# Kernel optimization log

Hardware: AMD Instinct MI355X
Metric: run time of the kernel (lower is better)

Reference implementation:

```python
import jax, jax.numpy as jnp
import numpy as np

B, T, V, D = 64, 128, 50000, 1024  # batch, num_steps, vocab_size, size


def setup_inputs() -> dict:
    key = jax.random.key(0)
    ks = jax.random.split(key, 5)
    inputs = jax.random.randint(ks[0], (B, T), 0, V, dtype=jnp.int32)
    input_lengths = jax.random.randint(ks[1], (B,), 0, T, dtype=jnp.int32)
    emb = jax.random.normal(ks[2], (V, D), dtype=jnp.float32) * 0.1  # ~truncated_normal(-0.1,0.1)
    # BasicLSTMCell weights: [input_dim + hidden, 4*hidden]
    W1 = jax.random.normal(ks[3], (2 * D, 4 * D), dtype=jnp.float32) / np.sqrt(2 * D)
    b1 = jnp.zeros((4 * D,), dtype=jnp.float32)
    W2 = jax.random.normal(ks[4], (2 * D, 4 * D), dtype=jnp.float32) / np.sqrt(2 * D)
    b2 = jnp.zeros((4 * D,), dtype=jnp.float32)
    return {"inputs": inputs, "input_lengths": input_lengths,
            "emb": emb, "W1": W1, "b1": b1, "W2": W2, "b2": b2}


def _lstm_cell(c, h, x, W, b):
    # BasicLSTMCell with forget_bias=0.0
    gates = jnp.concatenate([x, h], axis=-1) @ W + b  # [B, 4D]
    i, j, f, o = jnp.split(gates, 4, axis=-1)
    c_new = c * jax.nn.sigmoid(f) + jax.nn.sigmoid(i) * jnp.tanh(j)
    h_new = jnp.tanh(c_new) * jax.nn.sigmoid(o)
    return c_new, h_new


def reference(inputs, input_lengths, emb, W1, b1, W2, b2):
    # embedding_lookup on transposed inputs -> time-major [T, B, D]
    x_seq = jnp.transpose(emb[inputs], (1, 0, 2))
    # sequence_length semantics of tf rnn.rnn: past length, output is zero
    # and state is carried through unchanged.
    mask = (jnp.arange(T)[:, None] < input_lengths[None, :]).astype(emb.dtype)  # [T, B]

    def step(carry, xm):
        c1, h1, c2, h2 = carry
        x_t, m_t = xm
        m = m_t[:, None]  # [B, 1]
        c1n, h1n = _lstm_cell(c1, h1, x_t, W1, b1)
        c2n, h2n = _lstm_cell(c2, h2, h1n, W2, b2)
        c1 = m * c1n + (1.0 - m) * c1
        h1 = m * h1n + (1.0 - m) * h1
        c2 = m * c2n + (1.0 - m) * c2
        h2 = m * h2n + (1.0 - m) * h2
        out_t = h2n * m  # zero output past sequence end
        return (c1, h1, c2, h2), out_t

    zeros = jnp.zeros((B, D), dtype=emb.dtype)
    init = (zeros, zeros, zeros, zeros)
    _, outs = jax.lax.scan(step, init, (x_seq, mask))  # outs: [T, B, D]
    return outs.sum(axis=0)  # reduce_sum over time -> [B, D]
```

## Files before the change

kernel.cpp:

```cpp
#include <hip/hip_runtime.h>

#define B_ 64
#define T_ 128
#define D_ 1024
#define K2_ 2048
#define G_ 4096
#define SLOTW 65664

typedef __attribute__((ext_vector_type(8))) short bf16x8;
typedef __attribute__((ext_vector_type(4))) float f32x4;
typedef unsigned short u16;
typedef unsigned long long u64;

__device__ __forceinline__ u16 f2bf(float f) {
  unsigned int u = __float_as_uint(f);
  u += 0x7FFF + ((u >> 16) & 1);
  return (u16)(u >> 16);
}

__device__ __forceinline__ float fast_sigmoid(float x) {
  return 1.f / (1.f + __expf(-x));
}
__device__ __forceinline__ float fast_tanh(float x) {
  float e = __expf(-2.f * fabsf(x));
  float t = (1.f - e) / (1.f + e);
  return copysignf(t, x);
}

__device__ __forceinline__ void store4_wt(u16* addr, unsigned v) {
  asm volatile("global_store_dword %0, %1, off sc0 sc1"
               :: "v"((void*)addr), "v"(v) : "memory");
}

__device__ __forceinline__ void store_pair_wt(u16* base, size_t soff, u16 v, int tid) {
  unsigned other = __shfl_xor((unsigned)v, 1);
  if (!(tid & 1))
    store4_wt(base + soff, (unsigned)v | (other << 16));
}

__global__ __launch_bounds__(256) void transpose_w(const float* __restrict__ W,
                                                   u16* __restrict__ Wt) {
  __shared__ u16 tile[64][65];
  int bn = blockIdx.x & 63;
  int bk = blockIdx.x >> 6;
  int n0 = bn * 64, k0 = bk * 64;
  for (int i = threadIdx.x; i < 4096; i += 256) {
    int r = i >> 6, c = i & 63;
    tile[c][r] = f2bf(W[(size_t)(k0 + r) * G_ + n0 + c]);
  }
  __syncthreads();
  for (int i = threadIdx.x; i < 4096; i += 256) {
    int r = i >> 6, c = i & 63;
    Wt[(size_t)(n0 + r) * K2_ + k0 + c] = tile[r][c];
  }
}

__global__ __launch_bounds__(256) void gather_x(const int* __restrict__ inputs,
                                                const float* __restrict__ emb,
                                                u16* __restrict__ xg) {
  int idx = blockIdx.x * 256 + threadIdx.x;
  int d4 = idx & 255;
  int tb = idx >> 8;
  int t = tb >> 6, b = tb & 63;
  int tok = inputs[b * T_ + t];
  float4 v = ((const float4*)(emb + (size_t)tok * D_))[d4];
  u64 pk = (u64)f2bf(v.x)
         | ((u64)f2bf(v.y) << 16)
         | ((u64)f2bf(v.z) << 32)
         | ((u64)f2bf(v.w) << 48);
  *(u64*)(xg + (size_t)tb * D_ + d4 * 4) = pk;
}

__global__ void zero_buf(uint4* p, int n) {
  int i = blockIdx.x * blockDim.x + threadIdx.x;
  if (i < n) p[i] = make_uint4(0u, 0u, 0u, 0u);
}

__device__ __forceinline__ void arrive_dev(int* bar, int lineBase, int lb) {
  int a = __hip_atomic_fetch_add(bar + (size_t)(lineBase + (lb & 7)) * 32, 1,
                                 __ATOMIC_RELAXED, __HIP_MEMORY_SCOPE_AGENT);
  if (a == 15) {
    int r = __hip_atomic_fetch_add(bar + (size_t)(lineBase + 8) * 32, 1,
                                   __ATOMIC_RELAXED, __HIP_MEMORY_SCOPE_AGENT);
    if (r == 7)
      __hip_atomic_store(bar + (size_t)(lineBase + 9) * 32, 1,
                         __ATOMIC_RELAXED, __HIP_MEMORY_SCOPE_AGENT);
  }
}
__device__ __forceinline__ void waitdone_dev(int* bar, int lineBase) {
  while (!__hip_atomic_load(bar + (size_t)(lineBase + 9) * 32,
                            __ATOMIC_RELAXED, __HIP_MEMORY_SCOPE_AGENT))
    __builtin_amdgcn_s_sleep(1);
}
#define LINEOF(L, i) (10 + ((L) * 129 + (i)) * 10)

__global__ __launch_bounds__(512, 2) void lstm_persist(
    const u16* wt1, const u16* wt2,
    const u16* __restrict__ xg,
    u16* h1buf, u16* h1n, u16* h2buf,
    const u16* __restrict__ zbuf,
    const float* __restrict__ b1, const float* __restrict__ b2,
    const int* __restrict__ lens, float* __restrict__ out,
    int* bar) {
  __shared__ __attribute__((aligned(16))) float part[8][64][36];
  __shared__ __attribute__((aligned(16))) float gsum[64][36];
  const int blk = blockIdx.x;
  const int L = blk >> 7;
  const int lb = blk & 127;
  const int rg = lb & 1;
  const int cg = lb >> 1;
  const int tid = threadIdx.x;
  const int lane = tid & 63;
  const int wv = tid >> 6;
  const int dc = lane & 15;
  const int kq = lane >> 4;

  const u16* wt = L ? wt2 : wt1;
  const float* bias = L ? b2 : b1;

  bf16x8 wreg[4][8];
  {
    const u16* wb = wt + (size_t)(cg * 16 + dc) * K2_ + wv * 256 + kq * 8;
    #pragma unroll
    for (int g = 0; g < 4; ++g)
      #pragma unroll
      for (int ks = 0; ks < 8; ++ks)
        wreg[g][ks] = *(const bf16x8*)(wb + (size_t)g * D_ * K2_ + ks * 32);
  }
  #pragma unroll
  for (int g = 0; g < 4; ++g)
    #pragma unroll
    for (int ks = 0; ks < 8; ++ks)
      asm volatile("" : "+v"(wreg[g][ks]));

  const int crow = tid >> 4;
  const int cdc = tid & 15;
  const int grow = rg * 32 + crow;
  const int dcol = cg * 16 + cdc;
  const int len_r = lens[grow];
  float bias_g[4];
  #pragma unroll
  for (int g = 0; g < 4; ++g) bias_g[g] = bias[g * D_ + dcol];
  float creg = 0.f, hreg = 0.f, outreg = 0.f;

  const int r0 = rg * 32 + (lane & 15);
  const int koff = (wv & 3) * 256 + kq * 8;

  __syncthreads();
  if (tid == 0) {
    int a = __hip_atomic_fetch_add(bar + (size_t)(blk & 7) * 32, 1,
                                   __ATOMIC_RELAXED, __HIP_MEMORY_SCOPE_AGENT);
    if (a == 31) {
      int r = __hip_atomic_fetch_add(bar + 8 * 32, 1,
                                     __ATOMIC_RELAXED, __HIP_MEMORY_SCOPE_AGENT);
      if (r == 7)
        __hip_atomic_store(bar + 9 * 32, 1,
                           __ATOMIC_RELAXED, __HIP_MEMORY_SCOPE_AGENT);
    }
    while (!__hip_atomic_load(bar + 9 * 32,
                              __ATOMIC_RELAXED, __HIP_MEMORY_SCOPE_AGENT))
      __builtin_amdgcn_s_sleep(1);
  }
  __syncthreads();
  __builtin_amdgcn_fence(__ATOMIC_ACQUIRE, "agent");

  for (int i = 0; i <= 128; ++i) {
    const bool active = L ? (i >= 1) : (i < 128);
    const int t = L ? i - 1 : i;
    if (active) {
      if (tid == 0) {
        if (L == 0) {
          if (i >= 1) waitdone_dev(bar, LINEOF(0, i - 1));
        } else {
          waitdone_dev(bar, LINEOF(0, i - 1));
          if (i >= 2) waitdone_dev(bar, LINEOF(1, i - 1));
        }
      }
      __syncthreads();

      const u16* xsrc; const u16* hsrc;
      u16* w_h1n = nullptr; u16* w_h1b = nullptr; u16* w_h2b = nullptr;
      if (L == 0) {
        xsrc = xg + (size_t)t * (B_ * D_);
        hsrc = (i == 0) ? zbuf : h1buf + (size_t)(i - 1) * SLOTW;
        w_h1n = h1n + (size_t)i * SLOTW;
        w_h1b = h1buf + (size_t)i * SLOTW;
      } else {
        xsrc = h1n + (size_t)(i - 1) * SLOTW;
        hsrc = (i <= 1) ? zbuf : h2buf + (size_t)(i - 2) * SLOTW;
        w_h2b = h2buf + (size_t)(i - 1) * SLOTW;
      }
      const u16* src = (wv < 4) ? xsrc : hsrc;
      const u16* a0p = src + (size_t)r0 * D_ + koff;

      f32x4 acc[2][4];
      #pragma unroll
      for (int rt = 0; rt < 2; ++rt)
        #pragma unroll
        for (int g = 0; g < 4; ++g)
          acc[rt][g] = (f32x4){0.f, 0.f, 0.f, 0.f};

      #pragma unroll
      for (int ks = 0; ks < 8; ++ks) {
        bf16x8 a0 = *(const bf16x8*)(a0p + ks * 32);
        bf16x8 a1 = *(const bf16x8*)(a0p + 16 * D_ + ks * 32);
        #pragma unroll
        for (int g = 0; g < 4; ++g) {
          acc[0][g] = __builtin_amdgcn_mfma_f32_16x16x32_bf16(a0, wreg[g][ks], acc[0][g], 0, 0, 0);
          acc[1][g] = __builtin_amdgcn_mfma_f32_16x16x32_bf16(a1, wreg[g][ks], acc[1][g], 0, 0, 0);
        }
      }

      #pragma unroll
      for (int rt = 0; rt < 2; ++rt)
        #pragma unroll
        for (int g = 0; g < 4; ++g)
          *(f32x4*)&part[wv][g * 16 + dc][rt * 16 + kq * 4] = acc[rt][g];
      __syncthreads();

      {
        const int rcol = tid >> 3;
        const int rrow = (tid & 7) * 4;
        f32x4 s = *(const f32x4*)&part[0][rcol][rrow];
        #pragma unroll
        for (int w = 1; w < 8; ++w) s += *(const f32x4*)&part[w][rcol][rrow];
        *(f32x4*)&gsum[rcol][rrow] = s;
      }
      __syncthreads();

      {
        float gi = gsum[cdc][crow] + bias_g[0];
        float gj = gsum[16 + cdc][crow] + bias_g[1];
        float gf = gsum[32 + cdc][crow] + bias_g[2];
        float go = gsum[48 + cdc][crow] + bias_g[3];
        float is = fast_sigmoid(gi);
        float fs = fast_sigmoid(gf);
        float os = fast_sigmoid(go);
        float jt = fast_tanh(gj);
        float c_new = creg * fs + is * jt;
        float h_new = fast_tanh(c_new) * os;
        bool m = t < len_r;
        if (m) { creg = c_new; hreg = h_new; }
        size_t soff = (size_t)grow * D_ + dcol;
        if (L == 0) {
          store_pair_wt(w_h1n, soff, f2bf(h_new), tid);
          store_pair_wt(w_h1b, soff, f2bf(hreg), tid);
        } else {
          store_pair_wt(w_h2b, soff, f2bf(hreg), tid);
          if (m) outreg += h_new;
        }
      }

      asm volatile("s_waitcnt vmcnt(0)" ::: "memory");
      __syncthreads();
      if (tid == 0 && !(L == 1 && i == 128))
        arrive_dev(bar, LINEOF(L, i), lb);
    }
  }
  if (L == 1) out[(size_t)grow * D_ + dcol] = outreg;
}

extern "C" void kernel_launch(void* const* d_in, const int* in_sizes, int n_in,
                              void* d_out, int out_size, void* d_ws, size_t ws_size,
                              hipStream_t stream) {
  const int* inputs  = (const int*)d_in[0];
  const int* lengths = (const int*)d_in[1];
  const float* emb   = (const float*)d_in[2];
  const float* W1    = (const float*)d_in[3];
  const float* b1    = (const float*)d_in[4];
  const float* W2    = (const float*)d_in[5];
  const float* b2    = (const float*)d_in[6];
  float* out = (float*)d_out;

  char* p = (char*)d_ws;
  u16* h1buf = (u16*)p; p += (size_t)T_ * SLOTW * 2;
  u16* h1n   = (u16*)p; p += (size_t)T_ * SLOTW * 2;
  u16* h2buf = (u16*)p; p += (size_t)T_ * SLOTW * 2;
  u16* xg    = (u16*)p; p += (size_t)T_ * B_ * D_ * 2;
  u16* zbuf  = (u16*)p; p += (size_t)B_ * D_ * 2;
  int* bar   = (int*)p; p += 2590 * 128;
  u16* wt1 = h1buf;
  u16* wt2 = h1n;

  hipLaunchKernelGGL(transpose_w, dim3(2048), dim3(256), 0, stream, W1, wt1);
  hipLaunchKernelGGL(transpose_w, dim3(2048), dim3(256), 0, stream, W2, wt2);
  hipLaunchKernelGGL(gather_x, dim3(8192), dim3(256), 0, stream, inputs, emb, xg);
  hipLaunchKernelGGL(zero_buf, dim3(113), dim3(256), 0, stream, (uint4*)zbuf, 28912);

  hipLaunchKernelGGL(lstm_persist, dim3(256), dim3(512), 0, stream,
                     wt1, wt2, xg, h1buf, h1n, h2buf, zbuf, b1, b2, lengths, out,
                     bar);
}
```

Measured before the change: 921.2 us.

## Replace global barrier tree with XCD-local counters and per-XCD byte flags

Each block now counts arrivals on a counter local to its XCD (read from the hardware XCC id register). The last arriver on each XCD writes a byte flag, and waiters poll one 64-bit word of flags masked by the XCDs that are populated. This replaces the two-level agent-scope atomic tree plus done flag that every step paid, aiming to cut cross-die atomic latency on the per-timestep critical path. It relies on the workgroup-scope atomic being coherent among blocks on the same XCD, and on the XCD population counts being stable after the initial barrier.

```diff
diff --git a/kernel.cpp b/kernel.cpp
--- a/kernel.cpp
+++ b/kernel.cpp
@@ -27,8 +27,18 @@
   return copysignf(t, x);
 }
 
+__device__ __forceinline__ int get_xcc_id() {
+  int x;
+  asm volatile("s_getreg_b32 %0, hwreg(HW_REG_XCC_ID)" : "=s"(x));
+  return x & 7;
+}
+
 __device__ __forceinline__ void store4_wt(u16* addr, unsigned v) {
   asm volatile("global_store_dword %0, %1, off sc0 sc1"
+               :: "v"((void*)addr), "v"(v) : "memory");
+}
+__device__ __forceinline__ void store1_wt(unsigned char* addr, unsigned v) {
+  asm volatile("global_store_byte %0, %1, off sc0 sc1"
                :: "v"((void*)addr), "v"(v) : "memory");
 }
 
@@ -76,23 +86,7 @@
   if (i < n) p[i] = make_uint4(0u, 0u, 0u, 0u);
 }
 
-__device__ __forceinline__ void arrive_dev(int* bar, int lineBase, int lb) {
-  int a = __hip_atomic_fetch_add(bar + (size_t)(lineBase + (lb & 7)) * 32, 1,
-                                 __ATOMIC_RELAXED, __HIP_MEMORY_SCOPE_AGENT);
-  if (a == 15) {
-    int r = __hip_atomic_fetch_add(bar + (size_t)(lineBase + 8) * 32, 1,
-                                   __ATOMIC_RELAXED, __HIP_MEMORY_SCOPE_AGENT);
-    if (r == 7)
-      __hip_atomic_store(bar + (size_t)(lineBase + 9) * 32, 1,
-                         __ATOMIC_RELAXED, __HIP_MEMORY_SCOPE_AGENT);
-  }
-}
-__device__ __forceinline__ void waitdone_dev(int* bar, int lineBase) {
-  while (!__hip_atomic_load(bar + (size_t)(lineBase + 9) * 32,
-                            __ATOMIC_RELAXED, __HIP_MEMORY_SCOPE_AGENT))
-    __builtin_amdgcn_s_sleep(1);
-}
-#define LINEOF(L, i) (10 + ((L) * 129 + (i)) * 10)
+#define LOCLINE(L, x, i) (26 + ((L) * 8 + (x)) * 128 + (i))
 
 __global__ __launch_bounds__(512, 2) void lstm_persist(
     const u16* wt1, const u16* wt2,
@@ -101,7 +95,7 @@
     const u16* __restrict__ zbuf,
     const float* __restrict__ b1, const float* __restrict__ b2,
     const int* __restrict__ lens, float* __restrict__ out,
-    int* bar) {
+    int* bar, unsigned char* flags) {
   __shared__ __attribute__((aligned(16))) float part[8][64][36];
   __shared__ __attribute__((aligned(16))) float gsum[64][36];
   const int blk = blockIdx.x;
@@ -114,6 +108,7 @@
   const int wv = tid >> 6;
   const int dc = lane & 15;
   const int kq = lane >> 4;
+  const int xcd = get_xcc_id();
 
   const u16* wt = L ? wt2 : wt1;
   const float* bias = L ? b2 : b1;
@@ -145,6 +140,10 @@
 
   const int r0 = rg * 32 + (lane & 15);
   const int koff = (wv & 3) * 256 + kq * 8;
+
+  if (tid == 0)
+    __hip_atomic_fetch_add(bar + (size_t)(10 + L * 8 + xcd) * 32, 1,
+                           __ATOMIC_RELAXED, __HIP_MEMORY_SCOPE_AGENT);
 
   __syncthreads();
   if (tid == 0) {
@@ -164,16 +163,42 @@
   __syncthreads();
   __builtin_amdgcn_fence(__ATOMIC_ACQUIRE, "agent");
 
+  u64 m0 = 0, m1 = 0;
+  int nloc = 0;
+  if (tid == 0) {
+    #pragma unroll
+    for (int x = 0; x < 8; ++x) {
+      int c0 = __hip_atomic_load(bar + (size_t)(10 + x) * 32,
+                                 __ATOMIC_RELAXED, __HIP_MEMORY_SCOPE_AGENT);
+      int c1 = __hip_atomic_load(bar + (size_t)(18 + x) * 32,
+                                 __ATOMIC_RELAXED, __HIP_MEMORY_SCOPE_AGENT);
+      if (c0) m0 |= 1ULL << (8 * x);
+      if (c1) m1 |= 1ULL << (8 * x);
+    }
+    nloc = __hip_atomic_load(bar + (size_t)(10 + L * 8 + xcd) * 32,
+                             __ATOMIC_RELAXED, __HIP_MEMORY_SCOPE_AGENT);
+  }
+
   for (int i = 0; i <= 128; ++i) {
     const bool active = L ? (i >= 1) : (i < 128);
     const int t = L ? i - 1 : i;
     if (active) {
-      if (tid == 0) {
+      if (tid == 0 && i >= 1) {
+        const u64* f = (const u64*)(flags + (size_t)(i - 1) * 128);
         if (L == 0) {
-          if (i >= 1) waitdone_dev(bar, LINEOF(0, i - 1));
+          while ((__hip_atomic_load(f, __ATOMIC_RELAXED,
+                                    __HIP_MEMORY_SCOPE_AGENT) & m0) != m0)
+            __builtin_amdgcn_s_sleep(1);
         } else {
-          waitdone_dev(bar, LINEOF(0, i - 1));
-          if (i >= 2) waitdone_dev(bar, LINEOF(1, i - 1));
+          const bool n1 = (i >= 2);
+          for (;;) {
+            u64 v0 = __hip_atomic_load(f, __ATOMIC_RELAXED, __HIP_MEMORY_SCOPE_AGENT);
+            u64 v1 = n1 ? __hip_atomic_load(f + 1, __ATOMIC_RELAXED,
+                                            __HIP_MEMORY_SCOPE_AGENT)
+                        : m1;
+            if ((v0 & m0) == m0 && (v1 & m1) == m1) break;
+            __builtin_amdgcn_s_sleep(1);
+          }
         }
       }
       __syncthreads();
@@ -253,8 +278,12 @@
 
       asm volatile("s_waitcnt vmcnt(0)" ::: "memory");
       __syncthreads();
-      if (tid == 0 && !(L == 1 && i == 128))
-        arrive_dev(bar, LINEOF(L, i), lb);
+      if (tid == 0 && !(L == 1 && i == 128)) {
+        int a = __hip_atomic_fetch_add(bar + (size_t)LOCLINE(L, xcd, i) * 32, 1,
+                                       __ATOMIC_RELAXED, __HIP_MEMORY_SCOPE_WORKGROUP);
+        if (a == nloc - 1)
+          store1_wt(flags + (size_t)i * 128 + L * 8 + xcd, 1u);
+      }
     }
   }
   if (L == 1) out[(size_t)grow * D_ + dcol] = outreg;
@@ -278,16 +307,17 @@
   u16* h2buf = (u16*)p; p += (size_t)T_ * SLOTW * 2;
   u16* xg    = (u16*)p; p += (size_t)T_ * B_ * D_ * 2;
   u16* zbuf  = (u16*)p; p += (size_t)B_ * D_ * 2;
-  int* bar   = (int*)p; p += 2590 * 128;
+  int* bar   = (int*)p; p += 2074 * 128;
+  unsigned char* flags = (unsigned char*)p; p += 128 * 128;
   u16* wt1 = h1buf;
   u16* wt2 = h1n;
 
   hipLaunchKernelGGL(transpose_w, dim3(2048), dim3(256), 0, stream, W1, wt1);
   hipLaunchKernelGGL(transpose_w, dim3(2048), dim3(256), 0, stream, W2, wt2);
   hipLaunchKernelGGL(gather_x, dim3(8192), dim3(256), 0, stream, inputs, emb, xg);
-  hipLaunchKernelGGL(zero_buf, dim3(113), dim3(256), 0, stream, (uint4*)zbuf, 28912);
+  hipLaunchKernelGGL(zero_buf, dim3(101), dim3(256), 0, stream, (uint4*)zbuf, 25808);
 
   hipLaunchKernelGGL(lstm_persist, dim3(256), dim3(512), 0, stream,
                      wt1, wt2, xg, h1buf, h1n, h2buf, zbuf, b1, b2, lengths, out,
-                     bar);
-}
+                     bar, flags);
+}
```

Measured after the change: 1.028 ms. +11.6%, slower.

## Replace hierarchical atomic barrier with per-wave byte flags and row-group waits

Applied to the files above, without the earlier changes.

Drops the per-step two-level atomic counter barrier. Each wave now writes one write-through byte flag when its work for a step is done. Consumers poll 64 u64 words per row group in parallel across a wavefront, and each block waits only on producers for its own row group (rg), not a whole-grid barrier. This removes serialized atomic arrival chains and the pre-arrive __syncthreads, in exchange for more polling traffic and weaker ordering, since each wave signals after only its own vmcnt drain.

```diff
diff --git a/kernel.cpp b/kernel.cpp
--- a/kernel.cpp
+++ b/kernel.cpp
@@ -12,6 +12,9 @@
 typedef unsigned short u16;
 typedef unsigned long long u64;
 
+#define FREADY 0x0101010101010101ULL
+#define FOFF(i, L, rg) ((((size_t)(i) * 2 + (L)) * 2 + (rg)) * 64)
+
 __device__ __forceinline__ u16 f2bf(float f) {
   unsigned int u = __float_as_uint(f);
   u += 0x7FFF + ((u >> 16) & 1);
@@ -29,6 +32,10 @@
 
 __device__ __forceinline__ void store4_wt(u16* addr, unsigned v) {
   asm volatile("global_store_dword %0, %1, off sc0 sc1"
+               :: "v"((void*)addr), "v"(v) : "memory");
+}
+__device__ __forceinline__ void store1_wt(unsigned char* addr, unsigned v) {
+  asm volatile("global_store_byte %0, %1, off sc0 sc1"
                :: "v"((void*)addr), "v"(v) : "memory");
 }
 
@@ -76,24 +83,6 @@
   if (i < n) p[i] = make_uint4(0u, 0u, 0u, 0u);
 }
 
-__device__ __forceinline__ void arrive_dev(int* bar, int lineBase, int lb) {
-  int a = __hip_atomic_fetch_add(bar + (size_t)(lineBase + (lb & 7)) * 32, 1,
-                                 __ATOMIC_RELAXED, __HIP_MEMORY_SCOPE_AGENT);
-  if (a == 15) {
-    int r = __hip_atomic_fetch_add(bar + (size_t)(lineBase + 8) * 32, 1,
-                                   __ATOMIC_RELAXED, __HIP_MEMORY_SCOPE_AGENT);
-    if (r == 7)
-      __hip_atomic_store(bar + (size_t)(lineBase + 9) * 32, 1,
-                         __ATOMIC_RELAXED, __HIP_MEMORY_SCOPE_AGENT);
-  }
-}
-__device__ __forceinline__ void waitdone_dev(int* bar, int lineBase) {
-  while (!__hip_atomic_load(bar + (size_t)(lineBase + 9) * 32,
-                            __ATOMIC_RELAXED, __HIP_MEMORY_SCOPE_AGENT))
-    __builtin_amdgcn_s_sleep(1);
-}
-#define LINEOF(L, i) (10 + ((L) * 129 + (i)) * 10)
-
 __global__ __launch_bounds__(512, 2) void lstm_persist(
     const u16* wt1, const u16* wt2,
     const u16* __restrict__ xg,
@@ -101,7 +90,7 @@
     const u16* __restrict__ zbuf,
     const float* __restrict__ b1, const float* __restrict__ b2,
     const int* __restrict__ lens, float* __restrict__ out,
-    int* bar) {
+    int* bar, unsigned char* flags) {
   __shared__ __attribute__((aligned(16))) float part[8][64][36];
   __shared__ __attribute__((aligned(16))) float gsum[64][36];
   const int blk = blockIdx.x;
@@ -164,16 +153,26 @@
   __syncthreads();
   __builtin_amdgcn_fence(__ATOMIC_ACQUIRE, "agent");
 
+  const u64* fbase = (const u64*)flags;
+
   for (int i = 0; i <= 128; ++i) {
     const bool active = L ? (i >= 1) : (i < 128);
     const int t = L ? i - 1 : i;
     if (active) {
-      if (tid == 0) {
-        if (L == 0) {
-          if (i >= 1) waitdone_dev(bar, LINEOF(0, i - 1));
-        } else {
-          waitdone_dev(bar, LINEOF(0, i - 1));
-          if (i >= 2) waitdone_dev(bar, LINEOF(1, i - 1));
+      if (wv == 0 && i >= 1) {
+        const u64* pA = fbase + FOFF(i - 1, 0, rg) + lane;
+        const u64* pB = fbase + FOFF(i - 1, 1, rg) + lane;
+        const bool needB = (L == 1 && i >= 2);
+        bool okA = false, okB = !needB;
+        for (;;) {
+          if (!okA)
+            okA = (__hip_atomic_load(pA, __ATOMIC_RELAXED,
+                                     __HIP_MEMORY_SCOPE_AGENT) == FREADY);
+          if (!okB)
+            okB = (__hip_atomic_load(pB, __ATOMIC_RELAXED,
+                                     __HIP_MEMORY_SCOPE_AGENT) == FREADY);
+          if (__all(okA && okB)) break;
+          __builtin_amdgcn_s_sleep(2);
         }
       }
       __syncthreads();
@@ -252,9 +251,10 @@
       }
 
       asm volatile("s_waitcnt vmcnt(0)" ::: "memory");
-      __syncthreads();
-      if (tid == 0 && !(L == 1 && i == 128))
-        arrive_dev(bar, LINEOF(L, i), lb);
+      if (lane == 0 && !(L == 1 && i == 128)) {
+        unsigned char* fb = flags + (FOFF(i, L, rg) + cg) * 8 + wv;
+        store1_wt(fb, 1u);
+      }
     }
   }
   if (L == 1) out[(size_t)grow * D_ + dcol] = outreg;
@@ -278,16 +278,17 @@
   u16* h2buf = (u16*)p; p += (size_t)T_ * SLOTW * 2;
   u16* xg    = (u16*)p; p += (size_t)T_ * B_ * D_ * 2;
   u16* zbuf  = (u16*)p; p += (size_t)B_ * D_ * 2;
-  int* bar   = (int*)p; p += 2590 * 128;
+  int* bar   = (int*)p; p += 2048;
+  unsigned char* flags = (unsigned char*)p; p += (size_t)512 * 64 * 8;
   u16* wt1 = h1buf;
   u16* wt2 = h1n;
 
   hipLaunchKernelGGL(transpose_w, dim3(2048), dim3(256), 0, stream, W1, wt1);
   hipLaunchKernelGGL(transpose_w, dim3(2048), dim3(256), 0, stream, W2, wt2);
   hipLaunchKernelGGL(gather_x, dim3(8192), dim3(256), 0, stream, inputs, emb, xg);
-  hipLaunchKernelGGL(zero_buf, dim3(113), dim3(256), 0, stream, (uint4*)zbuf, 28912);
+  hipLaunchKernelGGL(zero_buf, dim3(97), dim3(256), 0, stream, (uint4*)zbuf, 24704);
 
   hipLaunchKernelGGL(lstm_persist, dim3(256), dim3(512), 0, stream,
                      wt1, wt2, xg, h1buf, h1n, h2buf, zbuf, b1, b2, lengths, out,
-                     bar);
-}
+                     bar, flags);
+}
```

Measured after the change: 1.672 ms. +81.5%, slower.

## Split per-step barrier by row group to narrow inter-block dependencies

Applied to the files above, without the earlier changes.

Replaces the per-layer, per-step device-wide barrier (all 128 blocks of a layer) with separate barriers per row group (rg), each counting 64 blocks through an 8-way fan-in tree. Consumer blocks now wait only on producers of the same batch-row half, which is valid if each row group reads only its own rows of h. The goal is less barrier latency and skew on the serial recurrence. In exchange the barrier region and its zeroing grow, and correctness depends on the row groups being truly independent.

```diff
diff --git a/kernel.cpp b/kernel.cpp
--- a/kernel.cpp
+++ b/kernel.cpp
@@ -76,23 +76,13 @@
   if (i < n) p[i] = make_uint4(0u, 0u, 0u, 0u);
 }
 
-__device__ __forceinline__ void arrive_dev(int* bar, int lineBase, int lb) {
-  int a = __hip_atomic_fetch_add(bar + (size_t)(lineBase + (lb & 7)) * 32, 1,
-                                 __ATOMIC_RELAXED, __HIP_MEMORY_SCOPE_AGENT);
-  if (a == 15) {
-    int r = __hip_atomic_fetch_add(bar + (size_t)(lineBase + 8) * 32, 1,
-                                   __ATOMIC_RELAXED, __HIP_MEMORY_SCOPE_AGENT);
-    if (r == 7)
-      __hip_atomic_store(bar + (size_t)(lineBase + 9) * 32, 1,
-                         __ATOMIC_RELAXED, __HIP_MEMORY_SCOPE_AGENT);
-  }
-}
-__device__ __forceinline__ void waitdone_dev(int* bar, int lineBase) {
-  while (!__hip_atomic_load(bar + (size_t)(lineBase + 9) * 32,
-                            __ATOMIC_RELAXED, __HIP_MEMORY_SCOPE_AGENT))
+#define GRPBASE(L, rg, i) (16 + (((L) * 2 + (rg)) * 129 + (i)) * 9)
+
+__device__ __forceinline__ void poll_root(const int* bar, int base) {
+  while (__hip_atomic_load(bar + (size_t)(base + 8) * 32,
+                           __ATOMIC_RELAXED, __HIP_MEMORY_SCOPE_AGENT) < 8)
     __builtin_amdgcn_s_sleep(1);
 }
-#define LINEOF(L, i) (10 + ((L) * 129 + (i)) * 10)
 
 __global__ __launch_bounds__(512, 2) void lstm_persist(
     const u16* wt1, const u16* wt2,
@@ -168,12 +158,12 @@
     const bool active = L ? (i >= 1) : (i < 128);
     const int t = L ? i - 1 : i;
     if (active) {
-      if (tid == 0) {
+      if (tid == 0 && i >= 1) {
         if (L == 0) {
-          if (i >= 1) waitdone_dev(bar, LINEOF(0, i - 1));
+          poll_root(bar, GRPBASE(0, rg, i - 1));
         } else {
-          waitdone_dev(bar, LINEOF(0, i - 1));
-          if (i >= 2) waitdone_dev(bar, LINEOF(1, i - 1));
+          poll_root(bar, GRPBASE(0, rg, i - 1));
+          if (i >= 2) poll_root(bar, GRPBASE(1, rg, i - 1));
         }
       }
       __syncthreads();
@@ -253,8 +243,14 @@
 
       asm volatile("s_waitcnt vmcnt(0)" ::: "memory");
       __syncthreads();
-      if (tid == 0 && !(L == 1 && i == 128))
-        arrive_dev(bar, LINEOF(L, i), lb);
+      if (tid == 0 && !(L == 1 && i == 128)) {
+        int base = GRPBASE(L, rg, i);
+        int a = __hip_atomic_fetch_add(bar + (size_t)(base + (cg & 7)) * 32, 1,
+                                       __ATOMIC_RELAXED, __HIP_MEMORY_SCOPE_AGENT);
+        if (a == 7)
+          __hip_atomic_fetch_add(bar + (size_t)(base + 8) * 32, 1,
+                                 __ATOMIC_RELAXED, __HIP_MEMORY_SCOPE_AGENT);
+      }
     }
   }
   if (L == 1) out[(size_t)grow * D_ + dcol] = outreg;
@@ -278,14 +274,14 @@
   u16* h2buf = (u16*)p; p += (size_t)T_ * SLOTW * 2;
   u16* xg    = (u16*)p; p += (size_t)T_ * B_ * D_ * 2;
   u16* zbuf  = (u16*)p; p += (size_t)B_ * D_ * 2;
-  int* bar   = (int*)p; p += 2590 * 128;
+  int* bar   = (int*)p; p += (size_t)4672 * 128;
   u16* wt1 = h1buf;
   u16* wt2 = h1n;
 
   hipLaunchKernelGGL(transpose_w, dim3(2048), dim3(256), 0, stream, W1, wt1);
   hipLaunchKernelGGL(transpose_w, dim3(2048), dim3(256), 0, stream, W2, wt2);
   hipLaunchKernelGGL(gather_x, dim3(8192), dim3(256), 0, stream, inputs, emb, xg);
-  hipLaunchKernelGGL(zero_buf, dim3(113), dim3(256), 0, stream, (uint4*)zbuf, 28912);
+  hipLaunchKernelGGL(zero_buf, dim3(178), dim3(256), 0, stream, (uint4*)zbuf, 45568);
 
   hipLaunchKernelGGL(lstm_persist, dim3(256), dim3(512), 0, stream,
                      wt1, wt2, xg, h1buf, h1n, h2buf, zbuf, b1, b2, lengths, out,
```

Result: no change. 936.5 us (+1.7%).
